# Kernel optimization log

Measured on AMD Instinct MI355X. Metric: run time of the kernel, lower is better.

The kernel has to match this reference:

```python
import jax, jax.numpy as jnp
import numpy as np

B, M, A, NS, T = 256, 16, 4096, 1024, 64
DT = 0.001          # dt
DA = DT             # da == dt
REF_T = 0.004       # refractory period (s)
SYN_DELAY_BINS = 1  # floor(syn_delay / da)
N_NEUR = 500.0      # neurons per population (self.N)
A_GRID = jnp.linspace(0.0, A * DA, A + 1)[:-1]  # (A,) ages since last spike


def _get_plam(input_total, V_old, age, rp, amem, ft):
    # V_old: (B,M,K); input_total: (B,M,1); age broadcasts against (B,M,K)
    V_new = V_old + DA * (rp - V_old) * amem + DA * input_total
    V_new = jnp.where(age < REF_T, 0.0, V_new)
    lam = jnp.where(V_new == 0.0, 1e-8, jnp.exp(V_new - ft))  # firing intensity
    p = lam * DT
    Plam = jnp.where(p >= 0.01, 1.0 - jnp.exp(-p), p)
    return V_new, Plam, lam


def setup_inputs() -> dict:
    key = jax.random.key(0)
    ks = jax.random.split(key, 13)
    return {
        "x": jax.random.normal(ks[0], (B, M), jnp.float32),
        "V_t_old": jax.random.normal(ks[1], (B, M, A), jnp.float32),
        "logS_t_old": jax.random.normal(ks[2], (B, M, A), jnp.float32),
        "sampled_neuron_v": jax.random.normal(ks[3], (B, M, NS), jnp.float32),
        "sampled_neuron_lastfire": jax.random.uniform(ks[4], (B, M, NS), jnp.float32),
        "I_syn": jax.random.uniform(ks[5], (B, M, 1), jnp.float32),
        "amem": jax.random.uniform(ks[6], (M, 1), jnp.float32),
        "asyn": jax.random.uniform(ks[7], (M, 1), jnp.float32),
        "J": jax.random.normal(ks[8], (M, M), jnp.float32),
        "rp": jax.random.uniform(ks[9], (M, 1), jnp.float32),
        "ft": jax.random.uniform(ks[10], (M, 1), jnp.float32),
        "eps": jax.random.uniform(ks[11], (1,), jnp.float32),
        "Z_hist_est": jnp.clip(jax.random.uniform(ks[12], (B, M, A + T), jnp.float32), 1e-5, 1.0),
        "internal_clock": 32,
    }


def reference(x, V_t_old, logS_t_old, sampled_neuron_v, sampled_neuron_lastfire,
              I_syn, amem, asyn, J, rp, ft, eps, Z_hist_est, internal_clock):
    clk = int(internal_clock)
    # ---- synaptic current with exponential decay and delayed pop activity ----
    exp_syn = jnp.exp(-DT * asyn)  # (M,1)
    if clk > SYN_DELAY_BINS:
        Z_t_last = Z_hist_est[:, :, clk + A - SYN_DELAY_BINS - 1:clk + A - SYN_DELAY_BINS]
        I_syn = exp_syn * I_syn + (1.0 - exp_syn) * Z_t_last / DT
    # input_total: (B,M,1)
    input_total = jnp.einsum('bm,mn->bn', I_syn[:, :, 0], J)[:, :, None] + (x * eps)[:, :, None]

    # ---- population activity update ----
    Z_t = Z_hist_est[:, :, clk:clk + A][:, :, ::-1]          # (B,M,A), youngest age first
    Z_t_new = Z_hist_est[:, :, clk + A:clk + A + 1]          # (B,M,1)

    V_t_new, Plam, _ = _get_plam(input_total, V_t_old, A_GRID, rp, amem, ft)

    S_old = jnp.exp(logS_t_old)
    m_t = S_old * Z_t
    Zmacro = jnp.sum(m_t * Plam, axis=2, keepdims=True)
    mess = 1.0 - jnp.sum(m_t, axis=2, keepdims=True)
    v_t = (1.0 - S_old) * m_t
    num = jnp.sum(v_t * Plam, axis=2, keepdims=True)
    den = jnp.sum(v_t, axis=2, keepdims=True)
    lambda_t = jnp.where(den != 0.0, num / jnp.where(den == 0.0, 1.0, den), 0.0)  # nan -> 0
    Z = jnp.clip(Zmacro + lambda_t * mess, 0.0, 1.0)
    A_t = Z / DT
    var = Z / N_NEUR + 0.1 * DT / N_NEUR
    Z_nll = 0.5 * jnp.square(Z_t_new - Z) / var + 0.5 * jnp.log(var) + 0.5 * jnp.log(2.0 * 3.14)

    # ---- sampled-neuron spike likelihood ----
    snv_new, Plam_s, lam_s = _get_plam(input_total, sampled_neuron_v, sampled_neuron_lastfire, rp, amem, ft)
    ltdt = lam_s * DT
    lnPy = jnp.where(ltdt < 0.01, snv_new - ft + jnp.log(DT), jnp.log(Plam_s))
    lnP1_y = -ltdt

    return (A_t, Z, Z_nll, lnPy, lnP1_y, V_t_new, snv_new, I_syn)
```

## Files before the change

kernel.cpp:

```cpp
#include <hip/hip_runtime.h>

#define B_   256
#define M_   16
#define A_   4096
#define NS_  1024
#define T_   64
#define AT_  (A_ + T_)

static constexpr float DTc = 0.001f;
static constexpr float DAc = 0.001f;
static constexpr float LOG_DT = -6.907755278982137f;

static constexpr size_t OFF_AT    = 0;
static constexpr size_t OFF_Z     = 4096;
static constexpr size_t OFF_ZNLL  = 8192;
static constexpr size_t OFF_LNPY  = 12288;
static constexpr size_t OFF_LNP1Y = 12288 + 4194304;
static constexpr size_t OFF_VT    = 12288 + 2ull * 4194304;
static constexpr size_t OFF_SNV   = OFF_VT + 16777216ull;
static constexpr size_t OFF_ISYN  = OFF_SNV + 4194304ull;

static __device__ __forceinline__ float4 ld4(const float* p) {
    return *reinterpret_cast<const float4*>(p);
}

__global__ __launch_bounds__(256, 4) void lif_kernel(
    const float* __restrict__ x,
    const float* __restrict__ V_t_old,
    const float* __restrict__ logS_t_old,
    const float* __restrict__ snv_in,
    const float* __restrict__ snlf,
    const float* __restrict__ I_syn,
    const float* __restrict__ amem,
    const float* __restrict__ asyn,
    const float* __restrict__ J,
    const float* __restrict__ rp,
    const float* __restrict__ ft,
    const float* __restrict__ eps,
    const float* __restrict__ Z_hist,
    const int*   __restrict__ clk_ptr,
    float* __restrict__ out)
{
    const int row  = blockIdx.x;
    const int b    = row >> 4;
    const int m    = row & 15;
    const int tid  = threadIdx.x;
    const int lane = tid & 63;

    __shared__ float sh_red[4][4];

    const size_t rowA = (size_t)row * A_;
    const size_t rowS = (size_t)row * NS_;

    const int   clk  = *clk_ptr;
    const float xv   = x[row];
    const float ev   = eps[0];
    const float a_m  = amem[m];
    const float rp_m = rp[m];
    const float ft_m = ft[m];

    const size_t rowZ = (size_t)row * AT_;
    const float  ztn  = Z_hist[rowZ + clk + A_];

    float asy = 0.0f, Iold = 0.0f, Jv = 0.0f, zl = 0.0f;
    if (lane < M_) {
        asy  = asyn[lane];
        Iold = I_syn[b * M_ + lane];
        Jv   = J[lane * M_ + m];
        if (clk > 1) zl = Z_hist[(size_t)(b * M_ + lane) * AT_ + (clk + A_ - 2)];
    }
    __builtin_amdgcn_sched_barrier(0);

    const float* pV = V_t_old    + rowA + tid * 4;
    const float* pS = logS_t_old + rowA + tid * 4;
    const float4 vA = ld4(pV);          const float4 vB = ld4(pV + 1024);
    const float4 vC = ld4(pV + 2048);   const float4 vD = ld4(pV + 3072);
    const float4 sA = ld4(pS);          const float4 sB = ld4(pS + 1024);
    const float4 sC = ld4(pS + 2048);   const float4 sD = ld4(pS + 3072);
    const float4 n4  = ld4(snv_in + rowS + tid * 4);
    const float4 lf4 = ld4(snlf   + rowS + tid * 4);

    const bool  zal = ((clk & 3) == 0);
    const float* pZ = Z_hist + rowZ + (clk + A_ - 4 - tid * 4);
    float4 zA, zB, zC, zD;
    if (zal) {
        zA = ld4(pZ);          zB = ld4(pZ - 1024);
        zC = ld4(pZ - 2048);   zD = ld4(pZ - 3072);
    } else {
        zA = make_float4(pZ[0], pZ[1], pZ[2], pZ[3]);
        zB = make_float4(pZ[-1024], pZ[-1023], pZ[-1022], pZ[-1021]);
        zC = make_float4(pZ[-2048], pZ[-2047], pZ[-2046], pZ[-2045]);
        zD = make_float4(pZ[-3072], pZ[-3071], pZ[-3070], pZ[-3069]);
    }
    __builtin_amdgcn_sched_barrier(0);

    float In = Iold;
    if (clk > 1 && lane < M_) {
        const float es = expf(-DTc * asy);
        In = es * Iold + (1.0f - es) * zl / DTc;
    }
    if (tid == m) out[OFF_ISYN + row] = In;
    float t = (lane < M_) ? In * Jv : 0.0f;
#pragma unroll
    for (int off = 8; off > 0; off >>= 1) t += __shfl_xor(t, off, 16);
    const float inT = __shfl(t, 0, 64) + xv * ev;

    float sZm = 0.0f, sMt = 0.0f, sNum = 0.0f, sDen = 0.0f;

#define CHUNK(cidx, vc, sc, zc)                                                 \
    do {                                                                        \
        const int a0 = (cidx) * 1024 + tid * 4;                                 \
        const float vov[4]  = {vc.x, vc.y, vc.z, vc.w};                         \
        const float lsv[4]  = {sc.x, sc.y, sc.z, sc.w};                         \
        const float zrev[4] = {zc.w, zc.z, zc.y, zc.x};                         \
        float vres[4];                                                          \
        _Pragma("unroll")                                                       \
        for (int k = 0; k < 4; ++k) {                                           \
            const int a = a0 + k;                                               \
            float V = vov[k] + DAc * (rp_m - vov[k]) * a_m + DAc * inT;         \
            if (a < 4) V = 0.0f;                               \
            float lam  = (V == 0.0f) ? 1e-8f : expf(V - ft_m);                  \
            float p    = lam * DTc;                                             \
            float Plam = (p >= 0.01f) ? (1.0f - expf(-p)) : p;                  \
            float S    = expf(lsv[k]);                                          \
            float mt   = S * zrev[k];                                           \
            sZm += mt * Plam;                                                   \
            sMt += mt;                                                          \
            float v = (1.0f - S) * mt;                                          \
            sNum += v * Plam;                                                   \
            sDen += v;                                                          \
            vres[k] = V;                                                        \
        }                                                                       \
        *reinterpret_cast<float4*>(out + OFF_VT + rowA + a0) =                  \
            make_float4(vres[0], vres[1], vres[2], vres[3]);                    \
    } while (0)

    CHUNK(0, vA, sA, zA);
    CHUNK(1, vB, sB, zB);
    CHUNK(2, vC, sC, zC);
    CHUNK(3, vD, sD, zD);
#undef CHUNK

    {
        const float vv[4] = {n4.x, n4.y, n4.z, n4.w};
        const float lf[4] = {lf4.x, lf4.y, lf4.z, lf4.w};
        float vn[4], py[4], p1[4];
#pragma unroll
        for (int k = 0; k < 4; ++k) {
            float V = vv[k] + DAc * (rp_m - vv[k]) * a_m + DAc * inT;
            if (lf[k] < 0.004f) V = 0.0f;
            float lam  = (V == 0.0f) ? 1e-8f : expf(V - ft_m);
            float ltdt = lam * DTc;
            float Plam = (ltdt >= 0.01f) ? (1.0f - expf(-ltdt)) : ltdt;
            py[k] = (ltdt < 0.01f) ? (V - ft_m + LOG_DT) : logf(Plam);
            p1[k] = -ltdt;
            vn[k] = V;
        }
        const int s0 = tid * 4;
        *reinterpret_cast<float4*>(out + OFF_SNV   + rowS + s0) = make_float4(vn[0], vn[1], vn[2], vn[3]);
        *reinterpret_cast<float4*>(out + OFF_LNPY  + rowS + s0) = make_float4(py[0], py[1], py[2], py[3]);
        *reinterpret_cast<float4*>(out + OFF_LNP1Y + rowS + s0) = make_float4(p1[0], p1[1], p1[2], p1[3]);
    }

    float vals[4] = {sZm, sMt, sNum, sDen};
#pragma unroll
    for (int i = 0; i < 4; ++i) {
        float v = vals[i];
        for (int off = 32; off > 0; off >>= 1) v += __shfl_down(v, off, 64);
        vals[i] = v;
    }
    const int wave = tid >> 6;
    if (lane == 0) {
#pragma unroll
        for (int i = 0; i < 4; ++i) sh_red[wave][i] = vals[i];
    }
    __syncthreads();
    if (tid == 0) {
        float Zm  = sh_red[0][0] + sh_red[1][0] + sh_red[2][0] + sh_red[3][0];
        float sM  = sh_red[0][1] + sh_red[1][1] + sh_red[2][1] + sh_red[3][1];
        float num = sh_red[0][2] + sh_red[1][2] + sh_red[2][2] + sh_red[3][2];
        float den = sh_red[0][3] + sh_red[1][3] + sh_red[2][3] + sh_red[3][3];
        float mess  = 1.0f - sM;
        float lam_t = (den != 0.0f) ? (num / den) : 0.0f;
        float Z = Zm + lam_t * mess;
        Z = fminf(fmaxf(Z, 0.0f), 1.0f);
        float At  = Z / DTc;
        float var = Z / 500.0f + 0.1f * DTc / 500.0f;
        float d   = ztn - Z;
        float znll = 0.5f * (d * d) / var + 0.5f * logf(var) + 0.5f * logf(2.0f * 3.14f);
        out[OFF_AT   + row] = At;
        out[OFF_Z    + row] = Z;
        out[OFF_ZNLL + row] = znll;
    }
}

extern "C" void kernel_launch(void* const* d_in, const int* in_sizes, int n_in,
                              void* d_out, int out_size, void* d_ws, size_t ws_size,
                              hipStream_t stream) {
    lif_kernel<<<B_ * M_, 256, 0, stream>>>(
        (const float*)d_in[0],
        (const float*)d_in[1],
        (const float*)d_in[2],
        (const float*)d_in[3],
        (const float*)d_in[4],
        (const float*)d_in[5],
        (const float*)d_in[6],
        (const float*)d_in[7],
        (const float*)d_in[8],
        (const float*)d_in[9],
        (const float*)d_in[10],
        (const float*)d_in[11],
        (const float*)d_in[12],
        (const int*)  d_in[13],
        (float*)d_out);
}
```

Measured before the change: 307.4 us.

## Map one wavefront per row with a software-pipelined chunk loop

Instead of one 256-thread block per row, each wavefront now processes a whole row, with four rows per block and a quarter as many blocks. The row is walked in 16 chunks with a two-deep register prefetch of V, logS and Z. The final reduction uses only wave shuffles, which removes the shared-memory reduction and __syncthreads. The aim is less sync overhead and more memory-level parallelism per wave. In exchange, each wave does four times the serial work, which may hurt latency hiding on this memory-bound kernel.

Result: no change. 313.1 us (+1.9%).

```diff
diff --git a/kernel.cpp b/kernel.cpp
--- a/kernel.cpp
+++ b/kernel.cpp
@@ -20,8 +20,139 @@
 static constexpr size_t OFF_SNV   = OFF_VT + 16777216ull;
 static constexpr size_t OFF_ISYN  = OFF_SNV + 4194304ull;
 
-static __device__ __forceinline__ float4 ld4(const float* p) {
-    return *reinterpret_cast<const float4*>(p);
+typedef float v4f __attribute__((ext_vector_type(4)));
+
+static __device__ __forceinline__ v4f ldv(const float* p) {
+    return *reinterpret_cast<const v4f*>(p);
+}
+
+template<bool ZAL>
+static __device__ __forceinline__ void do_row(
+    const int row, const int lane, const int clk, const float inT,
+    const float a_m, const float rp_m, const float ft_m, const float ztn,
+    const float* __restrict__ V_t_old,
+    const float* __restrict__ logS_t_old,
+    const float* __restrict__ snv_in,
+    const float* __restrict__ snlf,
+    const float* __restrict__ Z_hist,
+    float* __restrict__ out)
+{
+    const size_t rowA = (size_t)row * A_;
+    const size_t rowS = (size_t)row * NS_;
+    const size_t rowZ = (size_t)row * AT_;
+
+    const float* pV  = V_t_old    + rowA + lane * 4;
+    const float* pS  = logS_t_old + rowA + lane * 4;
+    const float* pZb = Z_hist + rowZ + (clk + A_ - 4 - lane * 4);
+    float*       pO  = out + OFF_VT + rowA + lane * 4;
+
+#define LDZ(c) ([&]() -> v4f {                                                  \
+        const float* p_ = pZb - (c) * 256;                                      \
+        if constexpr (ZAL) { return ldv(p_); }                                  \
+        else { v4f z_; z_.x = p_[0]; z_.y = p_[1]; z_.z = p_[2]; z_.w = p_[3];  \
+               return z_; } }())
+
+    float sZm = 0.0f, sMt = 0.0f, sNum = 0.0f, sDen = 0.0f;
+
+    v4f va = ldv(pV),       sa = ldv(pS),       za = LDZ(0);
+    v4f vb = ldv(pV + 256), sb = ldv(pS + 256), zb = LDZ(1);
+
+#pragma unroll 1
+    for (int c = 0; c < 16; ++c) {
+        const v4f vc_ = va, sc_ = sa, zc_ = za;
+        va = vb; sa = sb; za = zb;
+        if (c + 2 < 16) {
+            vb = ldv(pV + (c + 2) * 256);
+            sb = ldv(pS + (c + 2) * 256);
+            zb = LDZ(c + 2);
+        }
+        const int a0 = c * 256 + lane * 4;
+        const float vov[4]  = {vc_.x, vc_.y, vc_.z, vc_.w};
+        const float lsv[4]  = {sc_.x, sc_.y, sc_.z, sc_.w};
+        const float zrev[4] = {zc_.w, zc_.z, zc_.y, zc_.x};
+        float vres[4];
+#pragma unroll
+        for (int k = 0; k < 4; ++k) {
+            const int a = a0 + k;
+            float V = vov[k] + DAc * (rp_m - vov[k]) * a_m + DAc * inT;
+            if (a < 4) V = 0.0f;
+            float lam  = (V == 0.0f) ? 1e-8f : expf(V - ft_m);
+            float p    = lam * DTc;
+            float Plam = (p >= 0.01f) ? (1.0f - expf(-p)) : p;
+            float S    = expf(lsv[k]);
+            float mt   = S * zrev[k];
+            sZm += mt * Plam;
+            sMt += mt;
+            float v = (1.0f - S) * mt;
+            sNum += v * Plam;
+            sDen += v;
+            vres[k] = V;
+        }
+        v4f vo; vo.x = vres[0]; vo.y = vres[1]; vo.z = vres[2]; vo.w = vres[3];
+        *reinterpret_cast<v4f*>(pO + c * 256) = vo;
+    }
+#undef LDZ
+
+    const float* pN = snv_in + rowS + lane * 4;
+    const float* pL = snlf   + rowS + lane * 4;
+    v4f n0 = ldv(pN), n1 = ldv(pN + 256), n2 = ldv(pN + 512), n3 = ldv(pN + 768);
+    v4f l0 = ldv(pL), l1 = ldv(pL + 256), l2 = ldv(pL + 512), l3 = ldv(pL + 768);
+
+    float vals[4] = {sZm, sMt, sNum, sDen};
+#pragma unroll
+    for (int i = 0; i < 4; ++i) {
+        float v = vals[i];
+        for (int off = 32; off > 0; off >>= 1) v += __shfl_down(v, off, 64);
+        vals[i] = v;
+    }
+    if (lane == 0) {
+        float Zm  = vals[0];
+        float sM  = vals[1];
+        float num = vals[2];
+        float den = vals[3];
+        float mess  = 1.0f - sM;
+        float lam_t = (den != 0.0f) ? (num / den) : 0.0f;
+        float Z = Zm + lam_t * mess;
+        Z = fminf(fmaxf(Z, 0.0f), 1.0f);
+        float At  = Z / DTc;
+        float var = Z / 500.0f + 0.1f * DTc / 500.0f;
+        float d   = ztn - Z;
+        float znll = 0.5f * (d * d) / var + 0.5f * logf(var) + 0.5f * logf(2.0f * 3.14f);
+        out[OFF_AT   + row] = At;
+        out[OFF_Z    + row] = Z;
+        out[OFF_ZNLL + row] = znll;
+    }
+
+#define NSQ(nq, lq, q)                                                          \
+    do {                                                                        \
+        const float vv[4] = {nq.x, nq.y, nq.z, nq.w};                           \
+        const float lf[4] = {lq.x, lq.y, lq.z, lq.w};                           \
+        float vn[4], py[4], p1[4];                                              \
+        _Pragma("unroll")                                                       \
+        for (int k = 0; k < 4; ++k) {                                           \
+            float V = vv[k] + DAc * (rp_m - vv[k]) * a_m + DAc * inT;           \
+            if (lf[k] < 0.004f) V = 0.0f;                      \
+            float lam  = (V == 0.0f) ? 1e-8f : expf(V - ft_m);                  \
+            float ltdt = lam * DTc;                                             \
+            float Plam = (ltdt >= 0.01f) ? (1.0f - expf(-ltdt)) : ltdt;         \
+            py[k] = (ltdt < 0.01f) ? (V - ft_m + LOG_DT) : logf(Plam);          \
+            p1[k] = -ltdt;                                                      \
+            vn[k] = V;                                                          \
+        }                                                                       \
+        const size_t s0 = rowS + (q) * 256 + lane * 4;                          \
+        v4f o0; o0.x = vn[0]; o0.y = vn[1]; o0.z = vn[2]; o0.w = vn[3];         \
+        v4f o1; o1.x = py[0]; o1.y = py[1]; o1.z = py[2]; o1.w = py[3];         \
+        v4f o2; o2.x = p1[0]; o2.y = p1[1]; o2.z = p1[2]; o2.w = p1[3];         \
+        *reinterpret_cast<v4f*>(out + OFF_SNV   + s0) = o0;                     \
+        *reinterpret_cast<v4f*>(out + OFF_LNPY  + s0) = o1;                     \
+        *reinterpret_cast<v4f*>(out + OFF_LNP1Y + s0) = o2;                     \
+    } while (0)
+
+    NSQ(n0, l0, 0);
+    NSQ(n1, l1, 1);
+    NSQ(n2, l2, 2);
+    NSQ(n3, l3, 3);
+#undef NSQ
 }
 
 __global__ __launch_bounds__(256, 4) void lif_kernel(
@@ -41,24 +172,18 @@
     const int*   __restrict__ clk_ptr,
     float* __restrict__ out)
 {
-    const int row  = blockIdx.x;
+    const int wid  = threadIdx.x >> 6;
+    const int lane = threadIdx.x & 63;
+    const int row  = blockIdx.x * 4 + wid;
     const int b    = row >> 4;
     const int m    = row & 15;
-    const int tid  = threadIdx.x;
-    const int lane = tid & 63;
-
-    __shared__ float sh_red[4][4];
-
-    const size_t rowA = (size_t)row * A_;
-    const size_t rowS = (size_t)row * NS_;
-
-    const int   clk  = *clk_ptr;
-    const float xv   = x[row];
-    const float ev   = eps[0];
-    const float a_m  = amem[m];
-    const float rp_m = rp[m];
-    const float ft_m = ft[m];
-
+
+    const int    clk  = *clk_ptr;
+    const float  xv   = x[row];
+    const float  ev   = eps[0];
+    const float  a_m  = amem[m];
+    const float  rp_m = rp[m];
+    const float  ft_m = ft[m];
     const size_t rowZ = (size_t)row * AT_;
     const float  ztn  = Z_hist[rowZ + clk + A_];
 
@@ -69,135 +194,30 @@
         Jv   = J[lane * M_ + m];
         if (clk > 1) zl = Z_hist[(size_t)(b * M_ + lane) * AT_ + (clk + A_ - 2)];
     }
-    __builtin_amdgcn_sched_barrier(0);
-
-    const float* pV = V_t_old    + rowA + tid * 4;
-    const float* pS = logS_t_old + rowA + tid * 4;
-    const float4 vA = ld4(pV);          const float4 vB = ld4(pV + 1024);
-    const float4 vC = ld4(pV + 2048);   const float4 vD = ld4(pV + 3072);
-    const float4 sA = ld4(pS);          const float4 sB = ld4(pS + 1024);
-    const float4 sC = ld4(pS + 2048);   const float4 sD = ld4(pS + 3072);
-    const float4 n4  = ld4(snv_in + rowS + tid * 4);
-    const float4 lf4 = ld4(snlf   + rowS + tid * 4);
-
-    const bool  zal = ((clk & 3) == 0);
-    const float* pZ = Z_hist + rowZ + (clk + A_ - 4 - tid * 4);
-    float4 zA, zB, zC, zD;
-    if (zal) {
-        zA = ld4(pZ);          zB = ld4(pZ - 1024);
-        zC = ld4(pZ - 2048);   zD = ld4(pZ - 3072);
-    } else {
-        zA = make_float4(pZ[0], pZ[1], pZ[2], pZ[3]);
-        zB = make_float4(pZ[-1024], pZ[-1023], pZ[-1022], pZ[-1021]);
-        zC = make_float4(pZ[-2048], pZ[-2047], pZ[-2046], pZ[-2045]);
-        zD = make_float4(pZ[-3072], pZ[-3071], pZ[-3070], pZ[-3069]);
-    }
-    __builtin_amdgcn_sched_barrier(0);
-
     float In = Iold;
     if (clk > 1 && lane < M_) {
         const float es = expf(-DTc * asy);
         In = es * Iold + (1.0f - es) * zl / DTc;
     }
-    if (tid == m) out[OFF_ISYN + row] = In;
+    if (lane == m) out[OFF_ISYN + row] = In;
     float t = (lane < M_) ? In * Jv : 0.0f;
 #pragma unroll
     for (int off = 8; off > 0; off >>= 1) t += __shfl_xor(t, off, 16);
     const float inT = __shfl(t, 0, 64) + xv * ev;
 
-    float sZm = 0.0f, sMt = 0.0f, sNum = 0.0f, sDen = 0.0f;
-
-#define CHUNK(cidx, vc, sc, zc)                                                 \
-    do {                                                                        \
-        const int a0 = (cidx) * 1024 + tid * 4;                                 \
-        const float vov[4]  = {vc.x, vc.y, vc.z, vc.w};                         \
-        const float lsv[4]  = {sc.x, sc.y, sc.z, sc.w};                         \
-        const float zrev[4] = {zc.w, zc.z, zc.y, zc.x};                         \
-        float vres[4];                                                          \
-        _Pragma("unroll")                                                       \
-        for (int k = 0; k < 4; ++k) {                                           \
-            const int a = a0 + k;                                               \
-            float V = vov[k] + DAc * (rp_m - vov[k]) * a_m + DAc * inT;         \
-            if (a < 4) V = 0.0f;                               \
-            float lam  = (V == 0.0f) ? 1e-8f : expf(V - ft_m);                  \
-            float p    = lam * DTc;                                             \
-            float Plam = (p >= 0.01f) ? (1.0f - expf(-p)) : p;                  \
-            float S    = expf(lsv[k]);                                          \
-            float mt   = S * zrev[k];                                           \
-            sZm += mt * Plam;                                                   \
-            sMt += mt;                                                          \
-            float v = (1.0f - S) * mt;                                          \
-            sNum += v * Plam;                                                   \
-            sDen += v;                                                          \
-            vres[k] = V;                                                        \
-        }                                                                       \
-        *reinterpret_cast<float4*>(out + OFF_VT + rowA + a0) =                  \
-            make_float4(vres[0], vres[1], vres[2], vres[3]);                    \
-    } while (0)
-
-    CHUNK(0, vA, sA, zA);
-    CHUNK(1, vB, sB, zB);
-    CHUNK(2, vC, sC, zC);
-    CHUNK(3, vD, sD, zD);
-#undef CHUNK
-
-    {
-        const float vv[4] = {n4.x, n4.y, n4.z, n4.w};
-        const float lf[4] = {lf4.x, lf4.y, lf4.z, lf4.w};
-        float vn[4], py[4], p1[4];
-#pragma unroll
-        for (int k = 0; k < 4; ++k) {
-            float V = vv[k] + DAc * (rp_m - vv[k]) * a_m + DAc * inT;
-            if (lf[k] < 0.004f) V = 0.0f;
-            float lam  = (V == 0.0f) ? 1e-8f : expf(V - ft_m);
-            float ltdt = lam * DTc;
-            float Plam = (ltdt >= 0.01f) ? (1.0f - expf(-ltdt)) : ltdt;
-            py[k] = (ltdt < 0.01f) ? (V - ft_m + LOG_DT) : logf(Plam);
-            p1[k] = -ltdt;
-            vn[k] = V;
-        }
-        const int s0 = tid * 4;
-        *reinterpret_cast<float4*>(out + OFF_SNV   + rowS + s0) = make_float4(vn[0], vn[1], vn[2], vn[3]);
-        *reinterpret_cast<float4*>(out + OFF_LNPY  + rowS + s0) = make_float4(py[0], py[1], py[2], py[3]);
-        *reinterpret_cast<float4*>(out + OFF_LNP1Y + rowS + s0) = make_float4(p1[0], p1[1], p1[2], p1[3]);
-    }
-
-    float vals[4] = {sZm, sMt, sNum, sDen};
-#pragma unroll
-    for (int i = 0; i < 4; ++i) {
-        float v = vals[i];
-        for (int off = 32; off > 0; off >>= 1) v += __shfl_down(v, off, 64);
-        vals[i] = v;
-    }
-    const int wave = tid >> 6;
-    if (lane == 0) {
-#pragma unroll
-        for (int i = 0; i < 4; ++i) sh_red[wave][i] = vals[i];
-    }
-    __syncthreads();
-    if (tid == 0) {
-        float Zm  = sh_red[0][0] + sh_red[1][0] + sh_red[2][0] + sh_red[3][0];
-        float sM  = sh_red[0][1] + sh_red[1][1] + sh_red[2][1] + sh_red[3][1];
-        float num = sh_red[0][2] + sh_red[1][2] + sh_red[2][2] + sh_red[3][2];
-        float den = sh_red[0][3] + sh_red[1][3] + sh_red[2][3] + sh_red[3][3];
-        float mess  = 1.0f - sM;
-        float lam_t = (den != 0.0f) ? (num / den) : 0.0f;
-        float Z = Zm + lam_t * mess;
-        Z = fminf(fmaxf(Z, 0.0f), 1.0f);
-        float At  = Z / DTc;
-        float var = Z / 500.0f + 0.1f * DTc / 500.0f;
-        float d   = ztn - Z;
-        float znll = 0.5f * (d * d) / var + 0.5f * logf(var) + 0.5f * logf(2.0f * 3.14f);
-        out[OFF_AT   + row] = At;
-        out[OFF_Z    + row] = Z;
-        out[OFF_ZNLL + row] = znll;
+    if ((clk & 3) == 0) {
+        do_row<true >(row, lane, clk, inT, a_m, rp_m, ft_m, ztn,
+                      V_t_old, logS_t_old, snv_in, snlf, Z_hist, out);
+    } else {
+        do_row<false>(row, lane, clk, inT, a_m, rp_m, ft_m, ztn,
+                      V_t_old, logS_t_old, snv_in, snlf, Z_hist, out);
     }
 }
 
 extern "C" void kernel_launch(void* const* d_in, const int* in_sizes, int n_in,
                               void* d_out, int out_size, void* d_ws, size_t ws_size,
                               hipStream_t stream) {
-    lif_kernel<<<B_ * M_, 256, 0, stream>>>(
+    lif_kernel<<<(B_ * M_) / 4, 256, 0, stream>>>(
         (const float*)d_in[0],
         (const float*)d_in[1],
         (const float*)d_in[2],
```
